# Kernel optimization log

Hardware: AMD Instinct MI355X
Metric: run time of the kernel (lower is better)

Reference implementation:

```python
import jax, jax.numpy as jnp
import numpy as np

HIDDEN = 1024

def setup_inputs() -> dict:
    key = jax.random.key(0)
    k1, k2, k3 = jax.random.split(key, 3)
    X = jax.random.normal(k1, (4, 4096, HIDDEN), dtype=jnp.float32)
    # nn.Linear(hidden, 3*hidden): weight [3h, h], bias [3h]
    W = jax.random.normal(k2, (3 * HIDDEN, HIDDEN), dtype=jnp.float32) / np.sqrt(HIDDEN)
    b = jax.random.normal(k3, (3 * HIDDEN,), dtype=jnp.float32) * 0.01
    return {"X": X, "W": W, "b": b}

def reference(X, W, b):
    h = X.shape[-1]
    QKV = jnp.einsum('bsh,oh->bso', X, W) + b  # [B,S,3h]
    Q, K, V = jnp.split(QKV, 3, axis=-1)
    scores = jnp.einsum('bqh,bkh->bqk', Q, K) / jnp.sqrt(jnp.float32(h))
    attn = jax.nn.softmax(scores, axis=-1)
    return jnp.einsum('bqk,bkh->bqh', attn, V)
```

## Files before the change

### kernel.cpp

```cpp
#include <hip/hip_runtime.h>
#include <hip/hip_bf16.h>

typedef unsigned short u16;
typedef _Float16 f16x8 __attribute__((ext_vector_type(8)));
typedef _Float16 f16x2 __attribute__((ext_vector_type(2)));
typedef float f32x4 __attribute__((ext_vector_type(4)));

#if __has_builtin(__builtin_amdgcn_exp2f)
#define EXP2F(x) __builtin_amdgcn_exp2f(x)
#else
#define EXP2F(x) exp2f(x)
#endif
#define FA_C32 0.045084220027780106f

__device__ __forceinline__ f32x4 mfma16h(f16x8 a, f16x8 b, f32x4 c) {
  return __builtin_amdgcn_mfma_f32_16x16x32_f16(a, b, c, 0, 0, 0);
}
__device__ __forceinline__ unsigned pk2h(float a, float b) {
  union { _Float16 h[2]; unsigned u; } x;
  x.h[0] = (_Float16)a; x.h[1] = (_Float16)b;
  return x.u;
}
__device__ __forceinline__ u16 h1(float a) {
  union { _Float16 h; u16 u; } x; x.h = (_Float16)a; return x.u;
}

#if __has_builtin(__builtin_amdgcn_fdot2)
__device__ __forceinline__ float fdot2_(f16x2 a, f16x2 b, float c) {
  return __builtin_amdgcn_fdot2(a, b, c, false);
}
#else
__device__ __forceinline__ float fdot2_(f16x2 a, f16x2 b, float c) {
  return c + (float)a[0] * (float)b[0] + (float)a[1] * (float)b[1];
}
#endif

typedef __attribute__((address_space(1))) const unsigned int gas_u32;
typedef __attribute__((address_space(3))) unsigned int las_u32;
__device__ __forceinline__ void gl_lds16(const u16* g, u16* l) {
  __builtin_amdgcn_global_load_lds((gas_u32*)g, (las_u32*)l, 16, 0, 0);
}

__global__ __launch_bounds__(256) void cast_f16_k(const float* __restrict__ src,
                                                  u16* __restrict__ dst, int n8) {
  int i = blockIdx.x * 256 + threadIdx.x;
  if (i >= n8) return;
  const float4* s4 = (const float4*)src;
  float4 a = s4[i * 2], b = s4[i * 2 + 1];
  uint4 o;
  o.x = pk2h(a.x, a.y); o.y = pk2h(a.z, a.w);
  o.z = pk2h(b.x, b.y); o.w = pk2h(b.z, b.w);
  ((uint4*)dst)[i] = o;
}

template <int K_, int EPI>
__global__ __launch_bounds__(512, 1) void gemm8p(
    const u16* __restrict__ A, const u16* __restrict__ B,
    const float* __restrict__ bias, u16* __restrict__ D0, u16* __restrict__ D1,
    u16* __restrict__ D2, float* __restrict__ Df, const int ldc,
    const size_t strA, const size_t strB, const size_t strC) {
  constexpr int NT = K_ / 64;
  static_assert(NT >= 4 && (NT % 2) == 0, "need even NT >= 4");
  __shared__ __align__(16) u16 As[2][2][128 * 64];
  __shared__ __align__(16) u16 Bs[2][2][128 * 64];
  __shared__ float lds_l[256];

  const int tid = threadIdx.x, lane = tid & 63, wid = tid >> 6;
  const int l15 = lane & 15, lhi = lane >> 4;
  const int m0 = blockIdx.x * 256, n0 = blockIdx.y * 256;
  const int wm = wid >> 2, wn = wid & 3;
  const u16* Ag = A + (size_t)blockIdx.z * strA;
  const u16* Bg = B + (size_t)blockIdx.z * strB;

  const int srow8 = lane >> 3;
  const int sblk = (lane & 7) ^ srow8;

#define STAGE_Q(BUF, G, GROW0, ST)                                        \
  gl_lds16((G) + (size_t)((GROW0) + wid * 8 + srow8) * K_ +               \
               (ST) * 64 + sblk * 8,                                      \
           (BUF) + (wid * 8) * 64)

#define BAR()                                                             \
  asm volatile("" ::: "memory");                                          \
  __builtin_amdgcn_s_barrier();                                           \
  asm volatile("" ::: "memory")

#define LGKM0()                                                           \
  asm volatile("s_waitcnt lgkmcnt(0)" ::: "memory");                      \
  __builtin_amdgcn_sched_barrier(0)

#define SB0() __builtin_amdgcn_sched_barrier(0)
#define VMC6() asm volatile("s_waitcnt vmcnt(6)" ::: "memory")
#define VMC0() asm volatile("s_waitcnt vmcnt(0)" ::: "memory")

#define RD_A(DST, PB, MH)                                                 \
  _Pragma("unroll") for (int mf = 0; mf < 4; ++mf)                        \
  _Pragma("unroll") for (int ks = 0; ks < 2; ++ks)                        \
    DST[mf][ks] = *(const f16x8*)((PB) + ((MH) * 64 + mf * 16 + l15) * 64 \
                                  + (((ks * 4 + lhi) ^ (l15 & 7)) * 8));

#define RD_B(DST, PB, BO, NH)                                             \
  _Pragma("unroll") for (int nf = 0; nf < 2; ++nf)                        \
  _Pragma("unroll") for (int ks = 0; ks < 2; ++ks)                        \
    DST[nf][ks] = *(const f16x8*)((PB) + ((BO) + (NH) * 32 + nf * 16 + l15) * 64 \
                                  + (((ks * 4 + lhi) ^ (l15 & 7)) * 8));

#define MM(AV, BV, MB, NB2)                                               \
  __builtin_amdgcn_s_setprio(1);                                          \
  _Pragma("unroll") for (int mf = 0; mf < 4; ++mf)                        \
  _Pragma("unroll") for (int nf = 0; nf < 2; ++nf)                        \
  _Pragma("unroll") for (int ks = 0; ks < 2; ++ks)                        \
    acc[(MB) * 4 + mf][(NB2) * 2 + nf] =                                  \
        mfma16h(AV[mf][ks], BV[nf][ks], acc[(MB) * 4 + mf][(NB2) * 2 + nf]); \
  __builtin_amdgcn_s_setprio(0);

#define SUMA(FR, MH8)                                                     \
  if (EPI == 1 && wn == 0) {                                              \
    _Pragma("unroll") for (int mf = 0; mf < 4; ++mf)                      \
    _Pragma("unroll") for (int ks = 0; ks < 2; ++ks) {                    \
      const f16x2* _pr = (const f16x2*)&FR[mf][ks];                       \
      _Pragma("unroll") for (int j = 0; j < 4; ++j)                       \
        lsa[MH8][mf] = fdot2_(_pr[j], ones2, lsa[MH8][mf]);               \
    }                                                                     \
  }

  f32x4 acc[8][4];
#pragma unroll
  for (int i = 0; i < 8; ++i)
#pragma unroll
    for (int j = 0; j < 4; ++j) acc[i][j] = 0.f;

  float lsa[2][4];
#pragma unroll
  for (int i = 0; i < 2; ++i)
#pragma unroll
    for (int j = 0; j < 4; ++j) lsa[i][j] = 0.f;
  const f16x2 ones2 = {(_Float16)1.0f, (_Float16)1.0f};

  const int bofs = (wn & 1) * 64;

  STAGE_Q(&As[0][0][0],    Ag, m0,       0);
  STAGE_Q(&As[0][0][4096], Ag, m0 + 64,  0);
  STAGE_Q(&As[0][1][0],    Ag, m0 + 128, 0);
  STAGE_Q(&As[0][1][4096], Ag, m0 + 192, 0);
  STAGE_Q(&Bs[0][0][0],    Bg, n0,       0);
  STAGE_Q(&Bs[0][0][4096], Bg, n0 + 64,  0);
  STAGE_Q(&Bs[0][1][0],    Bg, n0 + 128, 0);
  STAGE_Q(&Bs[0][1][4096], Bg, n0 + 192, 0);
  STAGE_Q(&As[1][0][0],    Ag, m0,       1);
  STAGE_Q(&As[1][1][0],    Ag, m0 + 128, 1);
  STAGE_Q(&Bs[1][0][0],    Bg, n0,       1);
  STAGE_Q(&Bs[1][0][4096], Bg, n0 + 64,  1);
  STAGE_Q(&Bs[1][1][0],    Bg, n0 + 128, 1);
  STAGE_Q(&Bs[1][1][4096], Bg, n0 + 192, 1);
  VMC6();
  BAR();

#pragma unroll 2
  for (int u = 0; u < NT; ++u) {
    const int d = u & 1;
    const u16* Apb = &As[d][wm][0];
    const u16* Bpb = &Bs[d][wn >> 1][0];
    f16x8 a0[4][2], a1[4][2], b0[2][2], b1[2][2];

    RD_A(a0, Apb, 0);
    RD_B(b0, Bpb, bofs, 0);
    if (u + 1 < NT) {
      STAGE_Q(&As[d ^ 1][0][4096], Ag, m0 + 64,  u + 1);
      STAGE_Q(&As[d ^ 1][1][4096], Ag, m0 + 192, u + 1);
    }
    BAR();
    LGKM0();
    MM(a0, b0, 0, 0);
    SUMA(a0, 0);
    SB0();
    BAR();

    RD_B(b1, Bpb, bofs, 1);
    if (u + 2 < NT) {
      STAGE_Q(&As[d][0][0], Ag, m0,       u + 2);
      STAGE_Q(&As[d][1][0], Ag, m0 + 128, u + 2);
    }
    BAR();
    LGKM0();
    MM(a0, b1, 0, 1);
    SB0();
    BAR();

    RD_A(a1, Apb, 1);
    if (u + 2 < NT) {
      STAGE_Q(&Bs[d][0][0],    Bg, n0,       u + 2);
      STAGE_Q(&Bs[d][0][4096], Bg, n0 + 64,  u + 2);
      STAGE_Q(&Bs[d][1][0],    Bg, n0 + 128, u + 2);
      STAGE_Q(&Bs[d][1][4096], Bg, n0 + 192, u + 2);
    }
    BAR();
    LGKM0();
    MM(a1, b1, 1, 1);
    SUMA(a1, 1);
    MM(a1, b0, 1, 0);
    SB0();
    if (u + 2 < NT) { VMC6(); }
    else if (u + 2 == NT) { VMC0(); }
    BAR();
  }
#undef STAGE_Q
#undef BAR
#undef LGKM0
#undef SB0
#undef VMC6
#undef VMC0
#undef RD_A
#undef RD_B
#undef MM
#undef SUMA

  if (EPI == 2) {
    float bv[4];
#pragma unroll
    for (int cf = 0; cf < 4; ++cf) bv[cf] = bias[n0 + wn * 64 + cf * 16 + l15];
    const int region = n0 >> 10;
    const int ncol0 = (n0 & 1023) + wn * 64;
    if (region < 2) {
      u16* dst = region ? D1 : D0;
#pragma unroll
      for (int rf = 0; rf < 8; ++rf) {
        const int m = m0 + wm * 128 + rf * 16 + lhi * 4;
#pragma unroll
        for (int r = 0; r < 4; ++r)
#pragma unroll
          for (int cf = 0; cf < 4; ++cf)
            dst[(size_t)(m + r) * 1024 + ncol0 + cf * 16 + l15] = h1(acc[rf][cf][r] + bv[cf]);
      }
    } else {
#pragma unroll
      for (int rf = 0; rf < 8; ++rf) {
        const int m = m0 + wm * 128 + rf * 16 + lhi * 4;
        const int bb = m >> 12, s = m & 4095;
#pragma unroll
        for (int cf = 0; cf < 4; ++cf) {
          const int dcol = ncol0 + cf * 16 + l15;
          uint2 v;
          v.x = pk2h(acc[rf][cf][0] + bv[cf], acc[rf][cf][1] + bv[cf]);
          v.y = pk2h(acc[rf][cf][2] + bv[cf], acc[rf][cf][3] + bv[cf]);
          *(uint2*)&D2[(size_t)(bb * 1024 + dcol) * 4096 + s] = v;
        }
      }
    }
  } else if (EPI == 0) {
#pragma unroll
    for (int rf = 0; rf < 8; ++rf) {
      const int m = m0 + wm * 128 + rf * 16 + lhi * 4;
#pragma unroll
      for (int r = 0; r < 4; ++r)
#pragma unroll
        for (int cf = 0; cf < 4; ++cf) {
          const int n = n0 + wn * 64 + cf * 16 + l15;
          float p = fminf(EXP2F(acc[rf][cf][r] * FA_C32), 60000.f);
          D0[(size_t)blockIdx.z * strC + (size_t)(m + r) * ldc + n] = h1(p);
        }
    }
  } else {
    if (wn == 0) {
#pragma unroll
      for (int mh = 0; mh < 2; ++mh)
#pragma unroll
        for (int mf = 0; mf < 4; ++mf) {
          float s = lsa[mh][mf];
          s += __shfl_xor(s, 16, 64);
          s += __shfl_xor(s, 32, 64);
          if (lhi == 0) lds_l[wm * 128 + mh * 64 + mf * 16 + l15] = s;
        }
    }
    __syncthreads();
#pragma unroll
    for (int rf = 0; rf < 8; ++rf) {
      const int m = m0 + wm * 128 + rf * 16 + lhi * 4;
#pragma unroll
      for (int r = 0; r < 4; ++r) {
        const float li = 1.0f / lds_l[wm * 128 + rf * 16 + lhi * 4 + r];
#pragma unroll
        for (int cf = 0; cf < 4; ++cf) {
          const int n = n0 + wn * 64 + cf * 16 + l15;
          Df[(size_t)blockIdx.z * strC + (size_t)(m + r) * ldc + n] = acc[rf][cf][r] * li;
        }
      }
    }
  }
}

extern "C" void kernel_launch(void* const* d_in, const int* in_sizes, int n_in,
                              void* d_out, int out_size, void* d_ws, size_t ws_size,
                              hipStream_t stream) {
  const float* X = (const float*)d_in[0];
  const float* W = (const float*)d_in[1];
  const float* b = (const float*)d_in[2];
  float* out = (float*)d_out;
  char* ws = (char*)d_ws;

  const size_t SB = (size_t)4096 * 4096 * 2;
  const size_t QB = (size_t)4096 * 1024 * 2;
  const size_t WFB = (size_t)3072 * 1024 * 2;
  int NB = 1;
  if (ws_size >= 4 * SB + WFB + 12 * QB) NB = 4;
  else if (ws_size >= 2 * SB + WFB + 12 * QB) NB = 2;

  u16* S  = (u16*)(ws);
  u16* Xf = (u16*)(ws);
  u16* Wf = (u16*)(ws + (size_t)NB * SB);
  u16* Qf = (u16*)(ws + (size_t)NB * SB + WFB);
  u16* Kf = (u16*)(ws + (size_t)NB * SB + WFB + 4 * QB);
  u16* Vt = (u16*)(ws + (size_t)NB * SB + WFB + 8 * QB);

  cast_f16_k<<<8192, 256, 0, stream>>>(X, Xf, 16777216 / 8);
  cast_f16_k<<<1536, 256, 0, stream>>>(W, Wf, 3145728 / 8);

  gemm8p<1024, 2><<<dim3(64, 12, 1), 512, 0, stream>>>(
      Xf, Wf, b, Qf, Kf, Vt, nullptr, 0, 0, 0, 0);

  const size_t strQ = (size_t)4096 * 1024;
  const size_t strS = (size_t)4096 * 4096;
  const size_t strV = (size_t)1024 * 4096;
  for (int g = 0; g < 4; g += NB) {
    const u16* Qg = Qf + (size_t)g * strQ;
    const u16* Kg = Kf + (size_t)g * strQ;
    const u16* Vg = Vt + (size_t)g * strV;
    float* Og = out + (size_t)g * strQ;
    gemm8p<1024, 0><<<dim3(16, 16, NB), 512, 0, stream>>>(
        Qg, Kg, nullptr, S, nullptr, nullptr, nullptr, 4096, strQ, strQ, strS);
    gemm8p<4096, 1><<<dim3(16, 4, NB), 512, 0, stream>>>(
        S, Vg, nullptr, nullptr, nullptr, nullptr, Og, 1024, strS, strV, strQ);
  }
}
```

Measured before the change: 391.8 us.

## Cut GEMM main-loop barriers and reuse one A fragment register set

Restructures the GEMM main loop from three barrier-separated phases per K-step into one compute block bracketed by two barriers. All B fragments are read up front, and a partial lgkmcnt(4) wait lets the first MFMA group start before every LDS read has returned. Global-to-LDS staging for step u+2 is batched after the closing barrier. The two A fragment arrays are merged into one reused array to cut register pressure. The change is meant to reduce barrier stalls and VGPR usage, at the cost of less interleaving between global loads and MFMA within an iteration.

```diff
diff --git a/kernel.cpp b/kernel.cpp
--- a/kernel.cpp
+++ b/kernel.cpp
@@ -84,6 +84,10 @@
   asm volatile("" ::: "memory");                                          \
   __builtin_amdgcn_s_barrier();                                           \
   asm volatile("" ::: "memory")
+
+#define LGKM4()                                                           \
+  asm volatile("s_waitcnt lgkmcnt(4)" ::: "memory");                      \
+  __builtin_amdgcn_sched_barrier(0)
 
 #define LGKM0()                                                           \
   asm volatile("s_waitcnt lgkmcnt(0)" ::: "memory");                      \
@@ -154,58 +158,53 @@
   STAGE_Q(&Bs[1][1][0],    Bg, n0 + 128, 1);
   STAGE_Q(&Bs[1][1][4096], Bg, n0 + 192, 1);
   VMC6();
-  BAR();
 
 #pragma unroll 2
   for (int u = 0; u < NT; ++u) {
     const int d = u & 1;
     const u16* Apb = &As[d][wm][0];
     const u16* Bpb = &Bs[d][wn >> 1][0];
-    f16x8 a0[4][2], a1[4][2], b0[2][2], b1[2][2];
-
-    RD_A(a0, Apb, 0);
+    f16x8 a[4][2], b0[2][2], b1[2][2];
+
+    BAR();
+    RD_A(a, Apb, 0);
     RD_B(b0, Bpb, bofs, 0);
+    SB0();
+    RD_B(b1, Bpb, bofs, 1);
+    SB0();
     if (u + 1 < NT) {
       STAGE_Q(&As[d ^ 1][0][4096], Ag, m0 + 64,  u + 1);
       STAGE_Q(&As[d ^ 1][1][4096], Ag, m0 + 192, u + 1);
     }
+    LGKM4();
+    MM(a, b0, 0, 0);
+    SUMA(a, 0);
+    LGKM0();
+    MM(a, b1, 0, 1);
+    SB0();
+    RD_A(a, Apb, 1);
+    SB0();
+    LGKM0();
+    MM(a, b1, 1, 1);
+    SUMA(a, 1);
+    MM(a, b0, 1, 0);
+    SB0();
     BAR();
-    LGKM0();
-    MM(a0, b0, 0, 0);
-    SUMA(a0, 0);
-    SB0();
-    BAR();
-
-    RD_B(b1, Bpb, bofs, 1);
     if (u + 2 < NT) {
       STAGE_Q(&As[d][0][0], Ag, m0,       u + 2);
       STAGE_Q(&As[d][1][0], Ag, m0 + 128, u + 2);
-    }
-    BAR();
-    LGKM0();
-    MM(a0, b1, 0, 1);
-    SB0();
-    BAR();
-
-    RD_A(a1, Apb, 1);
-    if (u + 2 < NT) {
       STAGE_Q(&Bs[d][0][0],    Bg, n0,       u + 2);
       STAGE_Q(&Bs[d][0][4096], Bg, n0 + 64,  u + 2);
       STAGE_Q(&Bs[d][1][0],    Bg, n0 + 128, u + 2);
       STAGE_Q(&Bs[d][1][4096], Bg, n0 + 192, u + 2);
-    }
-    BAR();
-    LGKM0();
-    MM(a1, b1, 1, 1);
-    SUMA(a1, 1);
-    MM(a1, b0, 1, 0);
-    SB0();
-    if (u + 2 < NT) { VMC6(); }
-    else if (u + 2 == NT) { VMC0(); }
-    BAR();
+      VMC6();
+    } else if (u + 2 == NT) {
+      VMC0();
+    }
   }
 #undef STAGE_Q
 #undef BAR
+#undef LGKM4
 #undef LGKM0
 #undef SB0
 #undef VMC6
```

After: 407.1 us. 3.9% more time.
